# Performance work log

Hardware: AMD Instinct MI355X
Metric: run time of the kernel (lower is better)

## Reference

```python
import jax, jax.numpy as jnp
import numpy as np

D_MODEL = 512
NUM_HEADS = 8
D_K = D_MODEL // NUM_HEADS  # 64
NUM_FEATURES = 256
EPS = 1e-6


def _ortho_gaussian(m, d, seed):
    """Orthogonal random features: stacked QR blocks, rows rescaled to chi(d) norms."""
    rng = np.random.default_rng(seed)
    blocks = []
    for _ in range(int(np.ceil(m / d))):
        q, _ = np.linalg.qr(rng.standard_normal((d, d)))
        blocks.append(q.T)
    omega = np.concatenate(blocks, axis=0)[:m]
    norms = np.linalg.norm(rng.standard_normal((m, d)), axis=1)
    return (omega * norms[:, None]).astype(np.float32)


def setup_inputs() -> dict:
    key = jax.random.key(0)
    ks = jax.random.split(key, 7)
    B, L = 4, 8192
    s = 1.0 / np.sqrt(D_MODEL)
    return {
        "Q": jax.random.normal(ks[0], (B, L, D_MODEL), jnp.float32),
        "K": jax.random.normal(ks[1], (B, L, D_MODEL), jnp.float32),
        "V": jax.random.normal(ks[2], (B, L, D_MODEL), jnp.float32),
        "Wq": jax.random.normal(ks[3], (D_MODEL, D_MODEL), jnp.float32) * s,
        "Wk": jax.random.normal(ks[4], (D_MODEL, D_MODEL), jnp.float32) * s,
        "Wv": jax.random.normal(ks[5], (D_MODEL, D_MODEL), jnp.float32) * s,
        "Wo": jax.random.normal(ks[6], (D_MODEL, D_MODEL), jnp.float32) * s,
        "omega": jnp.asarray(_ortho_gaussian(NUM_FEATURES, D_K, 42)),
    }


def _phi(x, omega):
    """FAVOR+ positive softmax-kernel features. x: [B,H,L,d], omega: [m,d] -> [B,H,L,m]."""
    x = x * (D_K ** -0.25)  # fold in 1/sqrt(d_k) softmax scaling
    proj = jnp.einsum('bhld,md->bhlm', x, omega)
    sq = 0.5 * jnp.sum(x * x, axis=-1, keepdims=True)
    # subtract per-position max over features for numerical stability
    stab = jnp.max(proj, axis=-1, keepdims=True)
    return jnp.exp(proj - sq - stab) * (NUM_FEATURES ** -0.5) + EPS


def _split_heads(x, W):
    B, L, _ = x.shape
    return (x @ W).reshape(B, L, NUM_HEADS, D_K).transpose(0, 2, 1, 3)  # [B,H,L,d]


def reference(Q, K, V, Wq, Wk, Wv, Wo, omega):
    q = _split_heads(Q, Wq)
    k = _split_heads(K, Wk)
    v = _split_heads(V, Wv)
    qp = _phi(q, omega)  # [B,H,L,m]
    kp = _phi(k, omega)  # [B,H,L,m]
    # linear attention: O(L*m*d) instead of O(L^2)
    kv = jnp.einsum('bhlm,bhld->bhmd', kp, v)           # [B,H,m,d]
    num = jnp.einsum('bhlm,bhmd->bhld', qp, kv)          # [B,H,L,d]
    ksum = jnp.sum(kp, axis=2)                            # [B,H,m]
    den = jnp.einsum('bhlm,bhm->bhl', qp, ksum)          # [B,H,L]
    out = num / (den[..., None] + EPS)
    B, H, L, d = out.shape
    out = out.transpose(0, 2, 1, 3).reshape(B, L, H * d)
    return out @ Wo
```

## Files before the change

kernel.cpp:

```cpp
#include <hip/hip_runtime.h>

typedef unsigned int u32;
typedef __attribute__((ext_vector_type(8))) short short8;
typedef __attribute__((ext_vector_type(4))) short short4v;
typedef __attribute__((ext_vector_type(2))) u32 u32x2;
typedef __attribute__((ext_vector_type(4))) float f32x4;

#define DM 512
#define NH 8
#define DK 64
#define NF 256
#define L_ 8192
#define SCALE 0.35355339059327373f
#define INVSQM 0.0625f
#define EPS_ 1e-6f

__device__ __forceinline__ float bf2f(short s){
  union { u32 u; float f; } x; x.u = ((u32)(unsigned short)s) << 16; return x.f;
}
__device__ __forceinline__ short f2bf(float f){
  union { float f; u32 u; } x; x.f = f;
  u32 r = (x.u + 0x7FFF + ((x.u >> 16) & 1)) >> 16;
  return (short)r;
}
__device__ __forceinline__ u32 cvtpk(float lo, float hi){
  u32 r;
  asm("v_cvt_pk_bf16_f32 %0, %1, %2" : "=v"(r) : "v"(lo), "v"(hi));
  return r;
}

typedef const __attribute__((address_space(1))) u32* gas_t;
typedef __attribute__((address_space(3))) u32* las_t;
__device__ __forceinline__ void gl_lds16(const void* g, void* l){
  __builtin_amdgcn_global_load_lds((gas_t)g, (las_t)l, 16, 0, 0);
}
__device__ __forceinline__ f32x4 mfma16(short8 a, short8 b, f32x4 c){
  return __builtin_amdgcn_mfma_f32_16x16x32_bf16(a, b, c, 0, 0, 0);
}
__device__ __forceinline__ short8 lds_read8(const void* base, int byteoff){
  return *reinterpret_cast<const short8*>((const char*)base + byteoff);
}

__global__ __launch_bounds__(256) void k_wt(const float* __restrict__ W0, const float* __restrict__ W1,
                                            const float* __restrict__ W2, const float* __restrict__ W3,
                                            short* __restrict__ Wt){
  int bid = blockIdx.x;
  int mat = bid >> 6;
  int tr = (bid >> 3) & 7, tc = bid & 7;
  const float* W = mat==0 ? W0 : mat==1 ? W1 : mat==2 ? W2 : W3;
  short* O = Wt + (size_t)mat*DM*DM;
  __shared__ __align__(16) short tl[64*72];
  int t = threadIdx.x;
  #pragma unroll
  for (int i=0;i<4;++i){
    int c = i*256 + t;
    int r = c >> 4, cc = c & 15;
    f32x4 v = *reinterpret_cast<const f32x4*>(W + (size_t)(tr*64+r)*DM + tc*64 + cc*4);
    u32x2 o; o[0] = cvtpk(v[0], v[1]); o[1] = cvtpk(v[2], v[3]);
    *reinterpret_cast<u32x2*>((char*)tl + r*144 + cc*8) = o;
  }
  __syncthreads();
  #pragma unroll
  for (int i=0;i<2;++i){
    int c = i*256 + t;
    int n = c >> 3, kc = c & 7;
    short8 v;
    #pragma unroll
    for (int q=0;q<8;++q) v[q] = tl[(kc*8+q)*72 + n];
    *reinterpret_cast<short8*>(O + (size_t)(tc*64+n)*DM + tr*64 + kc*8) = v;
  }
}

__global__ __launch_bounds__(256) void k_omc(const float* __restrict__ Om, short* __restrict__ omc){
  int i = blockIdx.x*256 + threadIdx.x;
  f32x4 v = *((const f32x4*)Om + i);
  u32x2 o; o[0] = cvtpk(v[0], v[1]); o[1] = cvtpk(v[2], v[3]);
  *((u32x2*)omc + i) = o;
}

__global__ __launch_bounds__(256) void k_gemm3(const float* __restrict__ Q, const float* __restrict__ K,
                                               const float* __restrict__ V, const short* __restrict__ wt,
                                               short* __restrict__ qh, short* __restrict__ kh,
                                               short* __restrict__ vT, int rbase){
  __shared__ __align__(16) short lA[128*64];
  __shared__ __align__(16) short lB[128*64];
  __shared__ __align__(16) short lC[128*136];
  const int mode = blockIdx.y;
  const float* A = mode==0 ? Q : mode==1 ? K : V;
  const short* Bt = wt + (size_t)mode*DM*DM;
  const int t = threadIdx.x;
  const int w = t >> 6, lane = t & 63;
  const int wr = w >> 1, wc = w & 1;
  const int bid = blockIdx.x;
  const int bmx = gridDim.x >> 5;
  const int j = bid >> 3;
  const int bm = (bid & 7)*bmx + (j >> 2);
  const int bn = j & 3;
  const int row0 = bm*128, n0 = bn*128;
  f32x4 acc[4][4] = {};
  for (int ks=0; ks<8; ++ks){
    const float* gA32 = A + (size_t)(rbase+row0)*DM + ks*64;
    #pragma unroll
    for (int rnd=0; rnd<8; ++rnd){
      int c = rnd*256 + t;
      int r = c >> 4, cc = c & 15;
      f32x4 v = *reinterpret_cast<const f32x4*>(gA32 + (size_t)r*DM + cc*4);
      u32x2 o; o[0] = cvtpk(v[0], v[1]); o[1] = cvtpk(v[2], v[3]);
      int po = cc*8;
      *reinterpret_cast<u32x2*>((char*)lA + r*128 + (po ^ ((r&7)<<4))) = o;
    }
    const char* gB = (const char*)(Bt + (size_t)n0*DM + ks*64);
    #pragma unroll
    for (int rnd=0; rnd<4; ++rnd){
      int d = (rnd*256 + t)*16;
      int r = d >> 7, po = d & 127;
      gl_lds16(gB + (size_t)r*(DM*2) + (po ^ ((r&7)<<4)), (char*)lB + rnd*4096 + w*1024);
    }
    __syncthreads();
    #pragma unroll
    for (int kk=0; kk<2; ++kk){
      int kb = (kk*32 + ((lane>>4)<<3))*2;
      short8 af[4], bfr[4];
      #pragma unroll
      for (int i=0;i<4;++i){
        int m = wr*64 + i*16 + (lane&15);
        af[i] = lds_read8(lA, m*128 + (kb ^ ((m&7)<<4)));
      }
      #pragma unroll
      for (int j2=0;j2<4;++j2){
        int n = wc*64 + j2*16 + (lane&15);
        bfr[j2] = lds_read8(lB, n*128 + (kb ^ ((n&7)<<4)));
      }
      #pragma unroll
      for (int i=0;i<4;++i)
        #pragma unroll
        for (int j2=0;j2<4;++j2)
          acc[i][j2] = mfma16(af[i], bfr[j2], acc[i][j2]);
    }
    __syncthreads();
  }
  #pragma unroll
  for (int i=0;i<4;++i)
    #pragma unroll
    for (int j2=0;j2<4;++j2)
      #pragma unroll
      for (int jj=0;jj<4;++jj){
        int row = wr*64 + i*16 + ((lane>>4)<<2) + jj;
        int col = wc*64 + j2*16 + (lane&15);
        lC[row*136 + col] = f2bf(acc[i][j2][jj]);
      }
  __syncthreads();
  const int b = row0 >> 13;
  const int l0 = row0 & 8191;
  if (mode < 2){
    short* Os = mode ? kh : qh;
    #pragma unroll
    for (int it=0; it<8; ++it){
      int p = it*256 + t;
      int row = p >> 4, c16 = p & 15;
      short8 v = *reinterpret_cast<const short8*>((char*)lC + row*272 + c16*16);
      int col0 = n0 + c16*8;
      int h = col0 >> 6, dv = col0 & 63;
      size_t off = ((size_t)(b*NH + h)*L_ + (l0+row))*DK + dv;
      *reinterpret_cast<short8*>(Os + off) = v;
    }
  } else {
    #pragma unroll
    for (int it=0; it<8; ++it){
      int p = it*256 + t;
      int col = p >> 4, lp = p & 15;
      short8 v;
      #pragma unroll
      for (int q=0;q<8;++q) v[q] = lC[(lp*8+q)*136 + col];
      int h = (n0+col) >> 6, dv = (n0+col) & 63;
      size_t off = ((size_t)(b*NH+h)*DK + dv)*L_ + l0 + lp*8;
      *reinterpret_cast<short8*>(vT + off) = v;
    }
  }
}

__global__ __launch_bounds__(256) void k_gemmO(const short* __restrict__ A, const short* __restrict__ Bt,
                                               float* __restrict__ Out, int rbase){
  __shared__ __align__(16) short lA[128*64];
  __shared__ __align__(16) short lB[128*64];
  const int t = threadIdx.x;
  const int w = t >> 6, lane = t & 63;
  const int wr = w >> 1, wc = w & 1;
  const int bid = blockIdx.x;
  const int bmx = gridDim.x >> 5;
  const int j = bid >> 3;
  const int bm = (bid & 7)*bmx + (j >> 2);
  const int bn = j & 3;
  const int row0 = bm*128, n0 = bn*128;
  f32x4 acc[4][4] = {};
  for (int ks=0; ks<8; ++ks){
    const char* gA = (const char*)(A + (size_t)(rbase+row0)*DM + ks*64);
    #pragma unroll
    for (int rnd=0; rnd<4; ++rnd){
      int d = (rnd*256 + t)*16;
      int r = d >> 7, po = d & 127;
      gl_lds16(gA + (size_t)r*(DM*2) + (po ^ ((r&7)<<4)), (char*)lA + rnd*4096 + w*1024);
    }
    const char* gB = (const char*)(Bt + (size_t)n0*DM + ks*64);
    #pragma unroll
    for (int rnd=0; rnd<4; ++rnd){
      int d = (rnd*256 + t)*16;
      int r = d >> 7, po = d & 127;
      gl_lds16(gB + (size_t)r*(DM*2) + (po ^ ((r&7)<<4)), (char*)lB + rnd*4096 + w*1024);
    }
    __syncthreads();
    #pragma unroll
    for (int kk=0; kk<2; ++kk){
      int kb = (kk*32 + ((lane>>4)<<3))*2;
      short8 af[4], bfr[4];
      #pragma unroll
      for (int i=0;i<4;++i){
        int m = wr*64 + i*16 + (lane&15);
        af[i] = lds_read8(lA, m*128 + (kb ^ ((m&7)<<4)));
      }
      #pragma unroll
      for (int j2=0;j2<4;++j2){
        int n = wc*64 + j2*16 + (lane&15);
        bfr[j2] = lds_read8(lB, n*128 + (kb ^ ((n&7)<<4)));
      }
      #pragma unroll
      for (int i=0;i<4;++i)
        #pragma unroll
        for (int j2=0;j2<4;++j2)
          acc[i][j2] = mfma16(af[i], bfr[j2], acc[i][j2]);
    }
    __syncthreads();
  }
  #pragma unroll
  for (int i=0;i<4;++i)
    #pragma unroll
    for (int j2=0;j2<4;++j2)
      #pragma unroll
      for (int jj=0;jj<4;++jj){
        int row = wr*64 + i*16 + ((lane>>4)<<2) + jj;
        int col = wc*64 + j2*16 + (lane&15);
        Out[(size_t)(row0+row)*DM + n0 + col] = acc[i][j2][jj];
      }
}

__global__ __launch_bounds__(512) void k_phik(const short* __restrict__ kh, const short* __restrict__ vT,
                                              const short* __restrict__ omega,
                                              float* __restrict__ kvp, float* __restrict__ ksp){
  __shared__ __align__(16) short lOm[256*64];
  __shared__ __align__(16) short lK[128*64];
  __shared__ __align__(16) short lV[64*128];
  __shared__ __align__(16) short lP[256*136];
  __shared__ float lSq[128];
  __shared__ float lKsP[8][256];
  const int t = threadIdx.x, w = t>>6, lane = t&63;
  const int bid = blockIdx.x;
  const int bh = bid >> 3, sp = bid & 7;
  const char* khb = (const char*)(kh + (size_t)bh*L_*DK);
  const char* vtb = (const char*)(vT + (size_t)bh*DK*L_);
  #pragma unroll
  for (int rnd=0; rnd<4; ++rnd){
    int d = (rnd*512 + t)*16;
    int r = d >> 7, po = d & 127;
    gl_lds16((const char*)omega + r*128 + (po ^ ((r&7)<<4)), (char*)lOm + rnd*8192 + w*1024);
  }
  f32x4 kv[4][2] = {};
  float ksa[16] = {};
  for (int c=0;c<8;++c){
    int l0 = sp*1024 + c*128;
    #pragma unroll
    for (int rnd=0; rnd<2; ++rnd){
      int d = (rnd*512 + t)*16;
      { int r = d>>7, po = d&127;
        gl_lds16(khb + (size_t)(l0+r)*128 + (po ^ ((r&7)<<4)), (char*)lK + rnd*8192 + w*1024); }
      { int r = d>>8, po = d&255;
        gl_lds16(vtb + (size_t)r*(L_*2) + (size_t)l0*2 + (po ^ ((r&15)<<4)), (char*)lV + rnd*8192 + w*1024); }
    }
    __syncthreads();
    {
      int row = t >> 2, part = t & 3;
      float ss = 0.f;
      #pragma unroll
      for (int hh=0; hh<2; ++hh){
        int cb = part*32 + hh*16;
        short8 v = lds_read8(lK, row*128 + (cb ^ ((row&7)<<4)));
        #pragma unroll
        for (int q=0;q<8;++q){ float f = bf2f(v[q]); ss += f*f; }
      }
      ss += __shfl_xor(ss, 1, 64);
      ss += __shfl_xor(ss, 2, 64);
      if (part==0) lSq[row] = 0.0625f * ss;
    }
    __syncthreads();
    f32x4 p[16] = {};
    #pragma unroll
    for (int kk=0;kk<2;++kk){
      int kb = (kk*32 + ((lane>>4)<<3))*2;
      int m = w*16 + (lane&15);
      short8 a = lds_read8(lK, m*128 + (kb ^ ((m&7)<<4)));
      #pragma unroll
      for (int ft=0; ft<16; ++ft){
        int n = ft*16 + (lane&15);
        short8 b = lds_read8(lOm, n*128 + (kb ^ ((n&7)<<4)));
        p[ft] = mfma16(a, b, p[ft]);
      }
    }
    float mj[4] = {-1e30f,-1e30f,-1e30f,-1e30f};
    #pragma unroll
    for (int ft=0; ft<16; ++ft)
      #pragma unroll
      for (int j=0;j<4;++j){ float pv = p[ft][j]*SCALE; p[ft][j]=pv; mj[j] = fmaxf(mj[j], pv); }
    #pragma unroll
    for (int j=0;j<4;++j){
      float v = mj[j];
      v = fmaxf(v, __shfl_xor(v,1,64)); v = fmaxf(v, __shfl_xor(v,2,64));
      v = fmaxf(v, __shfl_xor(v,4,64)); v = fmaxf(v, __shfl_xor(v,8,64));
      mj[j] = v;
    }
    float sqv[4];
    #pragma unroll
    for (int j=0;j<4;++j) sqv[j] = lSq[w*16 + ((lane>>4)<<2) + j];
    int llb = w*16 + ((lane>>4)<<2);
    #pragma unroll
    for (int ft=0; ft<16; ++ft){
      int feat = ft*16 + (lane&15);
      float e0, e1, e2, e3;
      {
        e0 = __expf(p[ft][0] - sqv[0] - mj[0]) * INVSQM + EPS_;
        e1 = __expf(p[ft][1] - sqv[1] - mj[1]) * INVSQM + EPS_;
        e2 = __expf(p[ft][2] - sqv[2] - mj[2]) * INVSQM + EPS_;
        e3 = __expf(p[ft][3] - sqv[3] - mj[3]) * INVSQM + EPS_;
      }
      ksa[ft] += (e0 + e1) + (e2 + e3);
      u32x2 pk; pk[0] = cvtpk(e0, e1); pk[1] = cvtpk(e2, e3);
      *reinterpret_cast<u32x2*>((char*)lP + feat*272 + llb*2) = pk;
    }
    __syncthreads();
    #pragma unroll
    for (int ks2=0; ks2<4; ++ks2){
      int kb = (ks2*32 + ((lane>>4)<<3))*2;
      short8 a[4], b[2];
      #pragma unroll
      for (int i=0;i<4;++i){
        int m = i*16 + (lane&15);
        a[i] = lds_read8(lV, m*256 + (kb ^ ((m&15)<<4)));
      }
      #pragma unroll
      for (int j=0;j<2;++j){
        int n = (2*w+j)*16 + (lane&15);
        b[j] = lds_read8(lP, n*272 + kb);
      }
      #pragma unroll
      for (int i=0;i<4;++i)
        #pragma unroll
        for (int j=0;j<2;++j)
          kv[i][j] = mfma16(a[i], b[j], kv[i][j]);
    }
    __syncthreads();
  }
  float* kvb = kvp + (size_t)bid*64*256;
  #pragma unroll
  for (int i=0;i<4;++i)
    #pragma unroll
    for (int j=0;j<2;++j)
      #pragma unroll
      for (int jj=0;jj<4;++jj){
        int dv = i*16 + ((lane>>4)<<2) + jj;
        int feat = (2*w+j)*16 + (lane&15);
        kvb[dv*256 + feat] = kv[i][j][jj];
      }
  #pragma unroll
  for (int ft=0; ft<16; ++ft){
    float v = ksa[ft];
    v += __shfl_xor(v, 16, 64);
    v += __shfl_xor(v, 32, 64);
    if (lane < 16) lKsP[w][ft*16 + lane] = v;
  }
  __syncthreads();
  if (t < 256){
    float s = 0.f;
    #pragma unroll
    for (int wv=0; wv<8; ++wv) s += lKsP[wv][t];
    ksp[(size_t)bid*256 + t] = s;
  }
}

__global__ __launch_bounds__(256) void k_red(const float* __restrict__ kvp, const float* __restrict__ ksp,
                                             short* __restrict__ kvb, float* __restrict__ ksum){
  int bid = blockIdx.x;
  int bh = bid >> 3, part = bid & 7;
  int t = threadIdx.x;
  const float* base = kvp + (size_t)bh*8*16384;
  short* ob = kvb + (size_t)bh*16384;
  for (int i=0;i<8;++i){
    int e = part*2048 + i*256 + t;
    float s = 0.f;
    #pragma unroll
    for (int sp2=0; sp2<8; ++sp2) s += base[(size_t)sp2*16384 + e];
    ob[e] = f2bf(s);
  }
  if (part == 0){
    const float* kb = ksp + (size_t)bh*8*256;
    float s2 = 0.f;
    #pragma unroll
    for (int sp2=0; sp2<8; ++sp2) s2 += kb[sp2*256 + t];
    ksum[bh*256 + t] = s2;
  }
}

__global__ __launch_bounds__(512, 4) void k_phiq(const short* __restrict__ qh, const short* __restrict__ kvb,
                                                 const float* __restrict__ ksum, const short* __restrict__ omega,
                                                 short* __restrict__ attn){
  __shared__ __align__(16) char smem[69632];
  short* bufA = (short*)smem;
  short* bufB = (short*)(smem + 32768);
  float* lSq  = (float*)(smem + 67584);
  float* lKs  = (float*)(smem + 68096);
  float* lDen = (float*)(smem + 69120);
  const int t = threadIdx.x, w = t>>6, lane = t&63;
  const int bid = blockIdx.x;
  const int bh = bid >> 6, lt = bid & 63;
  const int l0 = lt*128;
  const char* qb = (const char*)(qh + (size_t)bh*L_*DK);
  #pragma unroll
  for (int rnd=0; rnd<4; ++rnd){
    int d = (rnd*512 + t)*16;
    int r = d>>7, po = d&127;
    gl_lds16((const char*)omega + r*128 + (po ^ ((r&7)<<4)), (char*)bufA + rnd*8192 + w*1024);
  }
  #pragma unroll
  for (int rnd=0; rnd<2; ++rnd){
    int d = (rnd*512 + t)*16;
    int r = d>>7, po = d&127;
    gl_lds16(qb + (size_t)(l0+r)*128 + (po ^ ((r&7)<<4)), (char*)bufB + rnd*8192 + w*1024);
  }
  if (t < 256) lKs[t] = ksum[bh*256 + t];
  __syncthreads();
  {
    int row = t >> 2, part = t & 3;
    float ss = 0.f;
    #pragma unroll
    for (int hh=0; hh<2; ++hh){
      int cb = part*32 + hh*16;
      short8 v = lds_read8(bufB, row*128 + (cb ^ ((row&7)<<4)));
      #pragma unroll
      for (int q=0;q<8;++q){ float f = bf2f(v[q]); ss += f*f; }
    }
    ss += __shfl_xor(ss, 1, 64);
    ss += __shfl_xor(ss, 2, 64);
    if (part==0) lSq[row] = 0.0625f * ss;
  }
  __syncthreads();
  f32x4 p[16] = {};
  #pragma unroll
  for (int kk=0;kk<2;++kk){
    int kb = (kk*32 + ((lane>>4)<<3))*2;
    int m = w*16 + (lane&15);
    short8 a = lds_read8(bufB, m*128 + (kb ^ ((m&7)<<4)));
    #pragma unroll
    for (int ft=0; ft<16; ++ft){
      int n = ft*16 + (lane&15);
      short8 b = lds_read8(bufA, n*128 + (kb ^ ((n&7)<<4)));
      p[ft] = mfma16(a, b, p[ft]);
    }
  }
  float mj[4] = {-1e30f,-1e30f,-1e30f,-1e30f};
  #pragma unroll
  for (int ft=0;ft<16;++ft)
    #pragma unroll
    for (int j=0;j<4;++j){ float pv = p[ft][j]*SCALE; p[ft][j]=pv; mj[j]=fmaxf(mj[j],pv); }
  #pragma unroll
  for (int j=0;j<4;++j){
    float v = mj[j];
    v = fmaxf(v,__shfl_xor(v,1,64)); v = fmaxf(v,__shfl_xor(v,2,64));
    v = fmaxf(v,__shfl_xor(v,4,64)); v = fmaxf(v,__shfl_xor(v,8,64));
    mj[j] = v;
  }
  float sqv[4];
  #pragma unroll
  for (int j=0;j<4;++j) sqv[j] = lSq[w*16 + ((lane>>4)<<2) + j];
  __syncthreads();
  const char* kvg = (const char*)(kvb + (size_t)bh*16384);
  #pragma unroll
  for (int rnd=0; rnd<4; ++rnd){
    int d = (rnd*512 + t)*16;
    int r = d>>9, po = d&511;
    gl_lds16(kvg + (size_t)r*512 + (po ^ ((r&31)<<4)), (char*)bufA + rnd*8192 + w*1024);
  }
  float dpart[4] = {0.f,0.f,0.f,0.f};
  const int rb = w*16 + ((lane>>4)<<2);
  #pragma unroll
  for (int ft=0;ft<8;++ft){
    int feat = ft*16 + (lane&15);
    float ksf = lKs[feat];
    #pragma unroll
    for (int j=0;j<4;++j){
      float e = __expf(p[ft][j]-sqv[j]-mj[j])*INVSQM + EPS_;
      dpart[j] += e*ksf;
      bufB[(rb+j)*136 + feat] = f2bf(e);
    }
  }
  __syncthreads();
  f32x4 nc[4] = {};
  #pragma unroll
  for (int ks2=0; ks2<4; ++ks2){
    int kb = (ks2*32 + ((lane>>4)<<3))*2;
    int n = w*16 + (lane&15);
    short8 bfr = lds_read8(bufB, n*272 + kb);
    #pragma unroll
    for (int i=0;i<4;++i){
      int mi = i*16 + (lane&15);
      short8 a = lds_read8(bufA, mi*512 + (kb ^ ((mi&31)<<4)));
      nc[i] = mfma16(a, bfr, nc[i]);
    }
  }
  #pragma unroll
  for (int ft=8;ft<16;++ft){
    int feat = ft*16 + (lane&15);
    float ksf = lKs[feat];
    #pragma unroll
    for (int j=0;j<4;++j){
      float e = __expf(p[ft][j]-sqv[j]-mj[j])*INVSQM + EPS_;
      dpart[j] += e*ksf;
      bufB[(rb+j)*136 + (feat-128)] = f2bf(e);
    }
  }
  #pragma unroll
  for (int j=0;j<4;++j){
    float v = dpart[j];
    v += __shfl_xor(v,1,64); v += __shfl_xor(v,2,64);
    v += __shfl_xor(v,4,64); v += __shfl_xor(v,8,64);
    if ((lane&15)==0) lDen[rb + j] = v;
  }
  #pragma unroll
  for (int ks2=4; ks2<8; ++ks2){
    int kbt = (ks2*32 + ((lane>>4)<<3))*2;
    int n = w*16 + (lane&15);
    short8 bfr = lds_read8(bufB, n*272 + (kbt - 256));
    #pragma unroll
    for (int i=0;i<4;++i){
      int mi = i*16 + (lane&15);
      short8 a = lds_read8(bufA, mi*512 + (kbt ^ ((mi&31)<<4)));
      nc[i] = mfma16(a, bfr, nc[i]);
    }
  }
  const int b = bh >> 3, h = bh & 7;
  const int l = w*16 + (lane&15);
  float rden = 1.0f / (lDen[l] + EPS_);
  #pragma unroll
  for (int i=0;i<4;++i){
    u32x2 ov;
    ov[0] = cvtpk(nc[i][0]*rden, nc[i][1]*rden);
    ov[1] = cvtpk(nc[i][2]*rden, nc[i][3]*rden);
    size_t off = ((size_t)(b*L_ + l0 + l))*DM + h*DK + i*16 + ((lane>>4)<<2);
    *reinterpret_cast<u32x2*>(attn + off) = ov;
  }
}

extern "C" void kernel_launch(void* const* d_in, const int* in_sizes, int n_in,
                              void* d_out, int out_size, void* d_ws, size_t ws_size,
                              hipStream_t stream){
  const float* Q  = (const float*)d_in[0];
  const float* K  = (const float*)d_in[1];
  const float* V  = (const float*)d_in[2];
  const float* Wq = (const float*)d_in[3];
  const float* Wk = (const float*)d_in[4];
  const float* Wv = (const float*)d_in[5];
  const float* Wo = (const float*)d_in[6];
  const float* Om = (const float*)d_in[7];
  char* ws = (char*)d_ws;

  short* wt  = (short*)(ws);
  short* omc = (short*)(ws + 2097152);

  k_wt<<<256, 256, 0, stream>>>(Wq, Wk, Wv, Wo, wt);
  k_omc<<<16, 256, 0, stream>>>(Om, omc);

  const size_t MONO_NEED = 120946688ull;
  if (ws_size >= MONO_NEED){
    short* qh   = (short*)(ws + 2162688);
    short* kh   = (short*)(ws + 35717120);
    short* vT   = (short*)(ws + 69271552);
    float* kvp  = (float*)(ws + 102825984);
    float* ksp  = (float*)(ws + 119603200);
    short* kvb  = (short*)(ws + 119865344);
    float* ksum = (float*)(ws + 120913920);
    short* attn = kh;
    k_gemm3<<<dim3(1024,3), 256, 0, stream>>>(Q, K, V, wt, qh, kh, vT, 0);
    k_phik<<<256, 512, 0, stream>>>(kh, vT, omc, kvp, ksp);
    k_red<<<256, 256, 0, stream>>>(kvp, ksp, kvb, ksum);
    k_phiq<<<2048, 512, 0, stream>>>(qh, kvb, ksum, omc, attn);
    k_gemmO<<<1024, 256, 0, stream>>>(attn, wt + 786432, (float*)d_out, 0);
  } else {
    short* qh   = (short*)(ws + 2162688);
    short* kh   = (short*)(ws + 10551296);
    short* vT   = (short*)(ws + 18939904);
    float* kvp  = (float*)(ws + 27328512);
    float* ksp  = (float*)(ws + 31522816);
    short* kvb  = (short*)(ws + 31588352);
    float* ksum = (float*)(ws + 31850496);
    short* attn = kh;
    for (int b=0; b<4; ++b){
      int rbase = b*8192;
      k_gemm3<<<dim3(256,3), 256, 0, stream>>>(Q, K, V, wt, qh, kh, vT, rbase);
      k_phik<<<64, 512, 0, stream>>>(kh, vT, omc, kvp, ksp);
      k_red<<<64, 256, 0, stream>>>(kvp, ksp, kvb, ksum);
      k_phiq<<<512, 512, 0, stream>>>(qh, kvb, ksum, omc, attn);
      k_gemmO<<<256, 256, 0, stream>>>(attn, wt + 786432,
                                       (float*)d_out + (size_t)b*8192*DM, 0);
    }
  }
}
```

Measured before the change: 255.3 us.

## Double-buffer LDS tiles in projection GEMMs to overlap loads with MFMA

Both the QKV projection GEMM and the output projection GEMM now use ping-pong LDS buffers. The next k-slice is prefetched into the alternate buffer, through registers for the fp32 A operand and direct global-to-LDS loads for bf16 operands, while MFMAs run on the current slice. This removes one barrier per iteration and hides global load latency. The cost is 64KB of LDS per block, which may lower occupancy, plus extra registers for the prefetched fp32 A values. Correctness depends on the gl_lds16 completion wait happening inside the single remaining barrier.

```diff
diff --git a/kernel.cpp b/kernel.cpp
--- a/kernel.cpp
+++ b/kernel.cpp
@@ -82,9 +82,8 @@
                                                const float* __restrict__ V, const short* __restrict__ wt,
                                                short* __restrict__ qh, short* __restrict__ kh,
                                                short* __restrict__ vT, int rbase){
-  __shared__ __align__(16) short lA[128*64];
-  __shared__ __align__(16) short lB[128*64];
-  __shared__ __align__(16) short lC[128*136];
+  __shared__ __align__(16) char smem[65536];
+  short* lC = (short*)smem;
   const int mode = blockIdx.y;
   const float* A = mode==0 ? Q : mode==1 ? K : V;
   const short* Bt = wt + (size_t)mode*DM*DM;
@@ -97,26 +96,52 @@
   const int bm = (bid & 7)*bmx + (j >> 2);
   const int bn = j & 3;
   const int row0 = bm*128, n0 = bn*128;
+  const float* gA32 = A + (size_t)(rbase+row0)*DM;
+  const char*  gB   = (const char*)(Bt + (size_t)n0*DM);
+  const int cA = t;
+  f32x4 av[8];
+  #pragma unroll
+  for (int rnd=0; rnd<8; ++rnd){
+    int c = rnd*256 + cA;
+    int r = c >> 4, cc = c & 15;
+    av[rnd] = *reinterpret_cast<const f32x4*>(gA32 + (size_t)r*DM + cc*4);
+  }
+  #pragma unroll
+  for (int rnd=0; rnd<8; ++rnd){
+    int c = rnd*256 + cA;
+    int r = c >> 4, cc = c & 15;
+    u32x2 o; o[0] = cvtpk(av[rnd][0], av[rnd][1]); o[1] = cvtpk(av[rnd][2], av[rnd][3]);
+    int po = cc*8;
+    *reinterpret_cast<u32x2*>(smem + r*128 + (po ^ ((r&7)<<4))) = o;
+  }
+  #pragma unroll
+  for (int rnd=0; rnd<4; ++rnd){
+    int d = (rnd*256 + t)*16;
+    int r = d >> 7, po = d & 127;
+    gl_lds16(gB + (size_t)r*(DM*2) + (po ^ ((r&7)<<4)), smem + 32768 + rnd*4096 + w*1024);
+  }
   f32x4 acc[4][4] = {};
   for (int ks=0; ks<8; ++ks){
-    const float* gA32 = A + (size_t)(rbase+row0)*DM + ks*64;
-    #pragma unroll
-    for (int rnd=0; rnd<8; ++rnd){
-      int c = rnd*256 + t;
-      int r = c >> 4, cc = c & 15;
-      f32x4 v = *reinterpret_cast<const f32x4*>(gA32 + (size_t)r*DM + cc*4);
-      u32x2 o; o[0] = cvtpk(v[0], v[1]); o[1] = cvtpk(v[2], v[3]);
-      int po = cc*8;
-      *reinterpret_cast<u32x2*>((char*)lA + r*128 + (po ^ ((r&7)<<4))) = o;
-    }
-    const char* gB = (const char*)(Bt + (size_t)n0*DM + ks*64);
-    #pragma unroll
-    for (int rnd=0; rnd<4; ++rnd){
-      int d = (rnd*256 + t)*16;
-      int r = d >> 7, po = d & 127;
-      gl_lds16(gB + (size_t)r*(DM*2) + (po ^ ((r&7)<<4)), (char*)lB + rnd*4096 + w*1024);
-    }
+    const int cur = ks & 1;
+    char* lA = smem + cur*16384;
+    char* lB = smem + 32768 + cur*16384;
+    char* lAn = smem + (cur^1)*16384;
+    char* lBn = smem + 32768 + (cur^1)*16384;
     __syncthreads();
+    if (ks < 7){
+      #pragma unroll
+      for (int rnd=0; rnd<8; ++rnd){
+        int c = rnd*256 + cA;
+        int r = c >> 4, cc = c & 15;
+        av[rnd] = *reinterpret_cast<const f32x4*>(gA32 + (size_t)r*DM + (ks+1)*64 + cc*4);
+      }
+      #pragma unroll
+      for (int rnd=0; rnd<4; ++rnd){
+        int d = (rnd*256 + t)*16;
+        int r = d >> 7, po = d & 127;
+        gl_lds16(gB + (size_t)r*(DM*2) + (ks+1)*128 + (po ^ ((r&7)<<4)), lBn + rnd*4096 + w*1024);
+      }
+    }
     #pragma unroll
     for (int kk=0; kk<2; ++kk){
       int kb = (kk*32 + ((lane>>4)<<3))*2;
@@ -137,8 +162,18 @@
         for (int j2=0;j2<4;++j2)
           acc[i][j2] = mfma16(af[i], bfr[j2], acc[i][j2]);
     }
-    __syncthreads();
-  }
+    if (ks < 7){
+      #pragma unroll
+      for (int rnd=0; rnd<8; ++rnd){
+        int c = rnd*256 + cA;
+        int r = c >> 4, cc = c & 15;
+        u32x2 o; o[0] = cvtpk(av[rnd][0], av[rnd][1]); o[1] = cvtpk(av[rnd][2], av[rnd][3]);
+        int po = cc*8;
+        *reinterpret_cast<u32x2*>(lAn + r*128 + (po ^ ((r&7)<<4))) = o;
+      }
+    }
+  }
+  __syncthreads();
   #pragma unroll
   for (int i=0;i<4;++i)
     #pragma unroll
@@ -181,8 +216,7 @@
 
 __global__ __launch_bounds__(256) void k_gemmO(const short* __restrict__ A, const short* __restrict__ Bt,
                                                float* __restrict__ Out, int rbase){
-  __shared__ __align__(16) short lA[128*64];
-  __shared__ __align__(16) short lB[128*64];
+  __shared__ __align__(16) char smem[65536];
   const int t = threadIdx.x;
   const int w = t >> 6, lane = t & 63;
   const int wr = w >> 1, wc = w & 1;
@@ -192,23 +226,32 @@
   const int bm = (bid & 7)*bmx + (j >> 2);
   const int bn = j & 3;
   const int row0 = bm*128, n0 = bn*128;
+  const char* gA = (const char*)(A + (size_t)(rbase+row0)*DM);
+  const char* gB = (const char*)(Bt + (size_t)n0*DM);
+  #pragma unroll
+  for (int rnd=0; rnd<4; ++rnd){
+    int d = (rnd*256 + t)*16;
+    int r = d >> 7, po = d & 127;
+    gl_lds16(gA + (size_t)r*(DM*2) + (po ^ ((r&7)<<4)), smem + rnd*4096 + w*1024);
+    gl_lds16(gB + (size_t)r*(DM*2) + (po ^ ((r&7)<<4)), smem + 32768 + rnd*4096 + w*1024);
+  }
   f32x4 acc[4][4] = {};
   for (int ks=0; ks<8; ++ks){
-    const char* gA = (const char*)(A + (size_t)(rbase+row0)*DM + ks*64);
-    #pragma unroll
-    for (int rnd=0; rnd<4; ++rnd){
-      int d = (rnd*256 + t)*16;
-      int r = d >> 7, po = d & 127;
-      gl_lds16(gA + (size_t)r*(DM*2) + (po ^ ((r&7)<<4)), (char*)lA + rnd*4096 + w*1024);
-    }
-    const char* gB = (const char*)(Bt + (size_t)n0*DM + ks*64);
-    #pragma unroll
-    for (int rnd=0; rnd<4; ++rnd){
-      int d = (rnd*256 + t)*16;
-      int r = d >> 7, po = d & 127;
-      gl_lds16(gB + (size_t)r*(DM*2) + (po ^ ((r&7)<<4)), (char*)lB + rnd*4096 + w*1024);
-    }
+    const int cur = ks & 1;
+    char* lA = smem + cur*16384;
+    char* lB = smem + 32768 + cur*16384;
+    char* lAn = smem + (cur^1)*16384;
+    char* lBn = smem + 32768 + (cur^1)*16384;
     __syncthreads();
+    if (ks < 7){
+      #pragma unroll
+      for (int rnd=0; rnd<4; ++rnd){
+        int d = (rnd*256 + t)*16;
+        int r = d >> 7, po = d & 127;
+        gl_lds16(gA + (size_t)r*(DM*2) + (ks+1)*128 + (po ^ ((r&7)<<4)), lAn + rnd*4096 + w*1024);
+        gl_lds16(gB + (size_t)r*(DM*2) + (ks+1)*128 + (po ^ ((r&7)<<4)), lBn + rnd*4096 + w*1024);
+      }
+    }
     #pragma unroll
     for (int kk=0; kk<2; ++kk){
       int kb = (kk*32 + ((lane>>4)<<3))*2;
@@ -229,7 +272,6 @@
         for (int j2=0;j2<4;++j2)
           acc[i][j2] = mfma16(af[i], bfr[j2], acc[i][j2]);
     }
-    __syncthreads();
   }
   #pragma unroll
   for (int i=0;i<4;++i)
```

New measurement: 282.5 us. 1.11x slower.
